# Kernel optimization log

Hardware: AMD Instinct MI355X
Metric: run time of the kernel (lower is better)

Reference implementation:

```python
import jax, jax.numpy as jnp
import numpy as np

# qshift_a: Kingsbury 10-tap Q-shift filters (sum(h0a) = sqrt(2)).
_H0A = np.array([0.0351638365171441, 0.0, -0.0883294244510729,
                 0.233890320607236, 0.760272369066126, 0.587518297723561,
                 0.0, -0.114301837144249, 0.0, 0.0], dtype=np.float64)
_H0B = _H0A[::-1].copy()
_ALT = (-1.0) ** np.arange(10)
_H1A = _H0B * _ALT            # highpass tree a
_H1B = _H1A[::-1].copy()
# synthesis filters (g0a = h0b, g0b = h0a, g1a = h1b, g1b = h1a)
G0A = _H0B.astype(np.float32)
G0B = _H0A.astype(np.float32)
G1A = _H1B.astype(np.float32)
G1B = _H1A.astype(np.float32)


def _reflect(x, minx, maxx):
    # dtcwt symmetric-extension index reflection (static, numpy)
    x = np.asarray(x, dtype=np.float64)
    rng = maxx - minx
    rng2 = 2.0 * rng
    mod = np.fmod(x - minx, rng2)
    normed = np.where(mod < 0, mod + rng2, mod)
    out = np.where(normed >= rng, rng2 - normed, normed) + minx
    return out.astype(np.int64)


def _colifilt(X, ha, hb):
    # X: (B, C, r, c) -> (B, C, 2r, c). ha, hb are 1-D numpy filters (static).
    m = ha.shape[0]
    m2 = m // 2
    assert m2 % 2 == 1, 'implemented for 10/14/18-tap qshift (m/2 odd)'
    b, ch, r, c = X.shape
    r2 = r // 2
    xe = _reflect(np.arange(-m2, r + m2), -0.5, r - 0.5)   # static indices
    t = np.arange(2, r + m - 1, 2)
    if float(np.sum(ha * hb)) > 0:
        ta, tb = t, t - 1
    else:
        ta, tb = t - 1, t
    Xa = X[:, :, xe[ta], :]   # (B, C, r/2 + m/2 - 1, c)
    Xb = X[:, :, xe[tb], :]
    hao, hae = ha[0::2], ha[1::2]
    hbo, hbe = hb[0::2], hb[1::2]

    def vconv(Z, h):
        # valid convolution along dim 2 (true conv: filter flipped)
        hf = h[::-1]
        out = Z[:, :, 0:r2, :] * float(hf[0])
        for k in range(1, m2):
            out = out + Z[:, :, k:k + r2, :] * float(hf[k])
        return out

    y = jnp.stack([vconv(Xb, hao), vconv(Xa, hbo),
                   vconv(Xb, hae), vconv(Xa, hbe)], axis=3)  # (B,C,r/2,4,c)
    return y.reshape(b, ch, 2 * r, c)


def _rowifilt(X, ha, hb):
    return jnp.swapaxes(_colifilt(jnp.swapaxes(X, 2, 3), ha, hb), 2, 3)


def _c2q(wr, wi):
    # complex pair of subbands -> real quad image. wr, wi: (B, C, 2, H, W) -> (B, C, 2H, 2W)
    w1r, w2r = wr[:, :, 0], wr[:, :, 1]
    w1i, w2i = wi[:, :, 0], wi[:, :, 1]
    x1 = w1r + w2r
    x2 = w1i + w2i
    x3 = w1i - w2i
    x4 = w2r - w1r
    b, c, h, w = x1.shape
    top = jnp.stack([x1, x2], axis=-1).reshape(b, c, h, 2 * w)
    bot = jnp.stack([x3, x4], axis=-1).reshape(b, c, h, 2 * w)
    y = jnp.stack([top, bot], axis=-2).reshape(b, c, 2 * h, 2 * w)
    return y * np.float32(1.0 / np.sqrt(2.0))


def setup_inputs() -> dict:
    key = jax.random.key(0)
    k1, k2, k3 = jax.random.split(key, 3)
    B, C, H, W = 8, 64, 128, 128
    Yl = jax.random.normal(k1, (B, C, H, W), dtype=jnp.float32)
    Yhr = jax.random.normal(k2, (B, C, 6, H // 2, W // 2), dtype=jnp.float32)
    Yhi = jax.random.normal(k3, (B, C, 6, H // 2, W // 2), dtype=jnp.float32)
    return {"Yl": Yl, "Yhr": Yhr, "Yhi": Yhi}


def reference(Yl, Yhr, Yhi):
    lh = _c2q(Yhr[:, :, 0:6:5], Yhi[:, :, 0:6:5])
    hl = _c2q(Yhr[:, :, 2:4:1], Yhi[:, :, 2:4:1])
    hh = _c2q(Yhr[:, :, 1:5:3], Yhi[:, :, 1:5:3])
    y1 = _rowifilt(Yl, G0B, G0A) + _rowifilt(hl, G1B, G1A)
    y2 = _rowifilt(lh, G0B, G0A) + _rowifilt(hh, G1B, G1A)
    return _colifilt(y1, G0B, G0A) + _colifilt(y2, G1B, G1A)
```

## Files before the change

kernel.cpp:

```cpp
#include <hip/hip_runtime.h>

#define NTHREADS 256

__device__ __forceinline__ int reflect128(int p) {
    p = (p < 0) ? (-p - 1) : p;
    p = (p >= 128) ? (255 - p) : p;
    return p;
}

__constant__ int   cs0[4] = {2, 1, 1, 0};
__constant__ int   cs1[4] = {1, 2, 0, 1};
__constant__ float cc0[4][3] = {
    { 0.760272369066126f, -0.0883294244510729f,  0.0351638365171441f},
    { 0.233890320607236f,  0.587518297723561f,  -0.114301837144249f},
    {-0.114301837144249f,  0.587518297723561f,   0.233890320607236f},
    { 0.0351638365171441f, -0.0883294244510729f, 0.760272369066126f}};
__constant__ float cc1[4][3] = {
    { 0.233890320607236f,  0.587518297723561f,  -0.114301837144249f},
    {-0.760272369066126f,  0.0883294244510729f, -0.0351638365171441f},
    {-0.0351638365171441f, 0.0883294244510729f, -0.760272369066126f},
    {-0.114301837144249f,  0.587518297723561f,   0.233890320607236f}};

__global__ __launch_bounds__(NTHREADS, 6)
void dtcwt_inv_kernel(const float* __restrict__ Yl,
                      const float* __restrict__ Yhr,
                      const float* __restrict__ Yhi,
                      float* __restrict__ out)
{
    const int tid   = threadIdx.x;
    const int ct    = blockIdx.x;
    const int rt    = blockIdx.y;
    const int plane = blockIdx.z;

    const int OR0 = rt * 64, OC0 = ct * 64;
    const int i0r = OR0 >> 2, i0c = OC0 >> 2;
    const int yrb = 2 * i0r - 4;
    const int icb = 2 * i0c - 4;

    const float* yl = Yl + (size_t)plane * (128 * 128);
    const float* hr = Yhr + (size_t)plane * 6 * 4096;
    const float* hi = Yhi + (size_t)plane * 6 * 4096;

    __shared__ float sLh[40][40];
    __shared__ float sHl[40][40];
    __shared__ float sHh[40][40];
    __shared__ float sYl[40][40];

    const float RS2 = 0.70710678118654752440f;

    for (int e = tid; e < 1600; e += NTHREADS) {
        const int t = e / 40;
        const int u = e - t * 40;
        const int r2 = reflect128(yrb + t);
        const int c2 = reflect128(icb + u);
        sYl[t][u] = yl[r2 * 128 + c2];
    }

    for (int e = tid; e < 400; e += NTHREADS) {
        const int t2 = e / 20;
        const int u2 = e - t2 * 20;
        const int ar = i0r - 2 + t2;
        const int ac = i0c - 2 + u2;
        const int oobr = (ar < 0) | (ar >= 64);
        const int oobc = (ac < 0) | (ac >= 64);
        const int r2 = oobr ? ((ar < 0) ? (-ar - 1) : (127 - ar)) : ar;
        const int c2 = oobc ? ((ac < 0) ? (-ac - 1) : (127 - ac)) : ac;
        const int off = r2 * 64 + c2;
        const float ar0 = hr[off], ar1 = hr[4096 + off], ar2 = hr[2 * 4096 + off];
        const float ar3 = hr[3 * 4096 + off], ar4 = hr[4 * 4096 + off], ar5 = hr[5 * 4096 + off];
        const float ai0 = hi[off], ai1 = hi[4096 + off], ai2 = hi[2 * 4096 + off];
        const float ai3 = hi[3 * 4096 + off], ai4 = hi[4 * 4096 + off], ai5 = hi[5 * 4096 + off];
#pragma unroll
        for (int dt = 0; dt < 2; ++dt) {
#pragma unroll
            for (int du = 0; du < 2; ++du) {
                const int p = dt ^ oobr;
                const int q = du ^ oobc;
                const float sA = (p & q) ? -RS2 : RS2;
                const float sB = (p & (q ^ 1)) ? -RS2 : RS2;
                float b0, b5, b2v, b3, b1, b4;
                if (p == q) { b0 = ar0; b5 = ar5; b2v = ar2; b3 = ar3; b1 = ar1; b4 = ar4; }
                else        { b0 = ai0; b5 = ai5; b2v = ai2; b3 = ai3; b1 = ai1; b4 = ai4; }
                const int t = 2 * t2 + dt, u = 2 * u2 + du;
                sLh[t][u] = sA * b0 + sB * b5;
                sHl[t][u] = sA * b2v + sB * b3;
                sHh[t][u] = sA * b1 + sB * b4;
            }
        }
    }
    __syncthreads();

    const int c  = tid & 63;
    const int g  = tid >> 6;
    const int jc = c & 3;
    const int q2 = c >> 2;
    const float a0  = cc0[jc][0], a1  = cc0[jc][1], a2  = cc0[jc][2];
    const float b0w = cc1[jc][0], b1w = cc1[jc][1], b2w = cc1[jc][2];
    const int ub0 = 2 * q2 + (jc & 1) + 2 * cs0[jc];
    const int ub1 = 2 * q2 + ((jc & 1) ^ 1) + 2 * cs1[jc];

    const int tb = 8 * g;
    float y1v[14], y2v[14];
#pragma unroll
    for (int k = 0; k < 14; ++k) {
        const int t = tb + 1 + k;
        y1v[k] = sYl[t][ub0] * a0  + sYl[t][ub0 + 2] * a1  + sYl[t][ub0 + 4] * a2
               + sHl[t][ub1] * b0w + sHl[t][ub1 + 2] * b1w + sHl[t][ub1 + 4] * b2w;
        y2v[k] = sLh[t][ub0] * a0  + sLh[t][ub0 + 2] * a1  + sLh[t][ub0 + 4] * a2
               + sHh[t][ub1] * b0w + sHh[t][ub1 + 2] * b1w + sHh[t][ub1 + 4] * b2w;
    }

    float* op = out + ((size_t)plane * 256 + OR0 + 16 * g) * 256 + OC0 + c;
#pragma unroll
    for (int j = 0; j < 4; ++j) {
        const int p0 = j & 1, p1 = p0 ^ 1;
        const int r0 = p0 + 2 * cs0[j];
        const int r1 = p1 + 2 * cs1[j];
        const float d0 = cc0[j][0], d1 = cc0[j][1], d2 = cc0[j][2];
        const float e0 = cc1[j][0], e1 = cc1[j][1], e2 = cc1[j][2];
#pragma unroll
        for (int mm = 0; mm < 4; ++mm) {
            const int k0 = 2 * mm + r0 - 1;
            const int k1 = 2 * mm + r1 - 1;
            const float acc = y1v[k0] * d0 + y1v[k0 + 2] * d1 + y1v[k0 + 4] * d2
                            + y2v[k1] * e0 + y2v[k1 + 2] * e1 + y2v[k1 + 4] * e2;
            op[(size_t)(4 * mm + j) * 256] = acc;
        }
    }
}

extern "C" void kernel_launch(void* const* d_in, const int* in_sizes, int n_in,
                              void* d_out, int out_size, void* d_ws, size_t ws_size,
                              hipStream_t stream) {
    const float* Yl  = (const float*)d_in[0];
    const float* Yhr = (const float*)d_in[1];
    const float* Yhi = (const float*)d_in[2];
    float* out = (float*)d_out;

    const int planes = in_sizes[0] / (128 * 128);
    dim3 grid(4, 4, planes);
    dtcwt_inv_kernel<<<grid, NTHREADS, 0, stream>>>(Yl, Yhr, Yhi, out);
}
```

Baseline: 262.0 us.

## Store staged tiles transposed in fp16 shared memory and remap block order

Staged input tiles now live in shared memory as fp16 and are stored transposed (column-major), so each thread can pull its column strip with wide 16-byte vector loads instead of many scalar reads. This halves the shared-memory footprint and cuts the number of LDS instructions. The 3D grid becomes a 1D grid with an XCD-aware swizzle of block indices to plane and tile. Rounding inputs to fp16 loses precision relative to the fp32 reference and may exceed tolerance.

```diff
diff --git a/kernel.cpp b/kernel.cpp
--- a/kernel.cpp
+++ b/kernel.cpp
@@ -1,4 +1,5 @@
 #include <hip/hip_runtime.h>
+#include <hip/hip_fp16.h>
 
 #define NTHREADS 256
 
@@ -27,10 +28,15 @@
                       const float* __restrict__ Yhi,
                       float* __restrict__ out)
 {
-    const int tid   = threadIdx.x;
-    const int ct    = blockIdx.x;
-    const int rt    = blockIdx.y;
-    const int plane = blockIdx.z;
+    const int tid = threadIdx.x;
+
+    const int bid  = blockIdx.x;
+    const int perx = gridDim.x >> 3;
+    const int gidx = (bid & 7) * perx + (bid >> 3);
+    const int plane = gidx >> 4;
+    const int tile  = gidx & 15;
+    const int ct = tile & 3;
+    const int rt = tile >> 2;
 
     const int OR0 = rt * 64, OC0 = ct * 64;
     const int i0r = OR0 >> 2, i0c = OC0 >> 2;
@@ -41,19 +47,19 @@
     const float* hr = Yhr + (size_t)plane * 6 * 4096;
     const float* hi = Yhi + (size_t)plane * 6 * 4096;
 
-    __shared__ float sLh[40][40];
-    __shared__ float sHl[40][40];
-    __shared__ float sHh[40][40];
-    __shared__ float sYl[40][40];
+    __shared__ __align__(16) __half sT[4][40][40];
 
     const float RS2 = 0.70710678118654752440f;
 
-    for (int e = tid; e < 1600; e += NTHREADS) {
-        const int t = e / 40;
-        const int u = e - t * 40;
-        const int r2 = reflect128(yrb + t);
-        const int c2 = reflect128(icb + u);
-        sYl[t][u] = yl[r2 * 128 + c2];
+    for (int e = tid; e < 800; e += NTHREADS) {
+        const int t2 = e / 40;
+        const int u  = e - t2 * 40;
+        const int cg = reflect128(icb + u);
+        const int ra = reflect128(yrb + 2 * t2);
+        const int rb = reflect128(yrb + 2 * t2 + 1);
+        const __half2 hv = __halves2half2(__float2half(yl[ra * 128 + cg]),
+                                          __float2half(yl[rb * 128 + cg]));
+        *(__half2*)&sT[0][u][2 * t2] = hv;
     }
 
     for (int e = tid; e < 400; e += NTHREADS) {
@@ -71,21 +77,25 @@
         const float ai0 = hi[off], ai1 = hi[4096 + off], ai2 = hi[2 * 4096 + off];
         const float ai3 = hi[3 * 4096 + off], ai4 = hi[4 * 4096 + off], ai5 = hi[5 * 4096 + off];
 #pragma unroll
-        for (int dt = 0; dt < 2; ++dt) {
+        for (int du = 0; du < 2; ++du) {
+            const int q = du ^ oobc;
+            __half lh[2], hl[2], hh[2];
 #pragma unroll
-            for (int du = 0; du < 2; ++du) {
+            for (int dt = 0; dt < 2; ++dt) {
                 const int p = dt ^ oobr;
-                const int q = du ^ oobc;
                 const float sA = (p & q) ? -RS2 : RS2;
                 const float sB = (p & (q ^ 1)) ? -RS2 : RS2;
                 float b0, b5, b2v, b3, b1, b4;
                 if (p == q) { b0 = ar0; b5 = ar5; b2v = ar2; b3 = ar3; b1 = ar1; b4 = ar4; }
                 else        { b0 = ai0; b5 = ai5; b2v = ai2; b3 = ai3; b1 = ai1; b4 = ai4; }
-                const int t = 2 * t2 + dt, u = 2 * u2 + du;
-                sLh[t][u] = sA * b0 + sB * b5;
-                sHl[t][u] = sA * b2v + sB * b3;
-                sHh[t][u] = sA * b1 + sB * b4;
+                lh[dt] = __float2half(sA * b0 + sB * b5);
+                hl[dt] = __float2half(sA * b2v + sB * b3);
+                hh[dt] = __float2half(sA * b1 + sB * b4);
             }
+            const int u = 2 * u2 + du, t0 = 2 * t2;
+            *(__half2*)&sT[1][u][t0] = __halves2half2(lh[0], lh[1]);
+            *(__half2*)&sT[2][u][t0] = __halves2half2(hl[0], hl[1]);
+            *(__half2*)&sT[3][u][t0] = __halves2half2(hh[0], hh[1]);
         }
     }
     __syncthreads();
@@ -94,20 +104,34 @@
     const int g  = tid >> 6;
     const int jc = c & 3;
     const int q2 = c >> 2;
-    const float a0  = cc0[jc][0], a1  = cc0[jc][1], a2  = cc0[jc][2];
-    const float b0w = cc1[jc][0], b1w = cc1[jc][1], b2w = cc1[jc][2];
     const int ub0 = 2 * q2 + (jc & 1) + 2 * cs0[jc];
     const int ub1 = 2 * q2 + ((jc & 1) ^ 1) + 2 * cs1[jc];
 
-    const int tb = 8 * g;
+    union H16 { float4 v[2]; __half h[16]; };
     float y1v[14], y2v[14];
 #pragma unroll
-    for (int k = 0; k < 14; ++k) {
-        const int t = tb + 1 + k;
-        y1v[k] = sYl[t][ub0] * a0  + sYl[t][ub0 + 2] * a1  + sYl[t][ub0 + 4] * a2
-               + sHl[t][ub1] * b0w + sHl[t][ub1 + 2] * b1w + sHl[t][ub1 + 4] * b2w;
-        y2v[k] = sLh[t][ub0] * a0  + sLh[t][ub0 + 2] * a1  + sLh[t][ub0 + 4] * a2
-               + sHh[t][ub1] * b0w + sHh[t][ub1 + 2] * b1w + sHh[t][ub1 + 4] * b2w;
+    for (int k = 0; k < 14; ++k) { y1v[k] = 0.0f; y2v[k] = 0.0f; }
+
+#pragma unroll
+    for (int d = 0; d < 3; ++d) {
+        const float ad = cc0[jc][d];
+        const float bd = cc1[jc][d];
+        const int u0 = ub0 + 2 * d;
+        const int u1 = ub1 + 2 * d;
+        H16 xa, xb, xc, xd;
+        const float4* pa = (const float4*)&sT[0][u0][8 * g];
+        const float4* pb = (const float4*)&sT[2][u1][8 * g];
+        const float4* pc = (const float4*)&sT[1][u0][8 * g];
+        const float4* pd = (const float4*)&sT[3][u1][8 * g];
+        xa.v[0] = pa[0]; xa.v[1] = pa[1];
+        xb.v[0] = pb[0]; xb.v[1] = pb[1];
+        xc.v[0] = pc[0]; xc.v[1] = pc[1];
+        xd.v[0] = pd[0]; xd.v[1] = pd[1];
+#pragma unroll
+        for (int k = 0; k < 14; ++k) {
+            y1v[k] += __half2float(xa.h[k + 1]) * ad + __half2float(xb.h[k + 1]) * bd;
+            y2v[k] += __half2float(xc.h[k + 1]) * ad + __half2float(xd.h[k + 1]) * bd;
+        }
     }
 
     float* op = out + ((size_t)plane * 256 + OR0 + 16 * g) * 256 + OC0 + c;
@@ -138,6 +162,6 @@
     float* out = (float*)d_out;
 
     const int planes = in_sizes[0] / (128 * 128);
-    dim3 grid(4, 4, planes);
+    dim3 grid(planes * 16, 1, 1);
     dtcwt_inv_kernel<<<grid, NTHREADS, 0, stream>>>(Yl, Yhr, Yhi, out);
 }
```

Result: slower. 277.9 us (+6.1%).

## Interleave subband tiles as float2 in LDS and remap blocks to 1D grid

Applied to the files above, without the earlier changes.

The four separate float LDS tiles become two float2 tiles, Yl paired with Lh and Hl paired with Hh. The filter stage can then fetch both operands with one 64-bit LDS read, halving the number of shared-memory load instructions. The grid is flattened to 1D, and block IDs are remapped with an XCD-style swizzle ((bid&7)*perx + bid>>3) so consecutive tiles of a plane land on the same XCD, which may improve L2 reuse. The remap assumes the block count is divisible by 8, and the float2 layout may change LDS bank conflict patterns.

```diff
diff --git a/kernel.cpp b/kernel.cpp
--- a/kernel.cpp
+++ b/kernel.cpp
@@ -27,10 +27,15 @@
                       const float* __restrict__ Yhi,
                       float* __restrict__ out)
 {
-    const int tid   = threadIdx.x;
-    const int ct    = blockIdx.x;
-    const int rt    = blockIdx.y;
-    const int plane = blockIdx.z;
+    const int tid = threadIdx.x;
+
+    const int bid  = blockIdx.x;
+    const int perx = gridDim.x >> 3;
+    const int gidx = (bid & 7) * perx + (bid >> 3);
+    const int plane = gidx >> 4;
+    const int tile  = gidx & 15;
+    const int ct = tile & 3;
+    const int rt = tile >> 2;
 
     const int OR0 = rt * 64, OC0 = ct * 64;
     const int i0r = OR0 >> 2, i0c = OC0 >> 2;
@@ -41,10 +46,8 @@
     const float* hr = Yhr + (size_t)plane * 6 * 4096;
     const float* hi = Yhi + (size_t)plane * 6 * 4096;
 
-    __shared__ float sLh[40][40];
-    __shared__ float sHl[40][40];
-    __shared__ float sHh[40][40];
-    __shared__ float sYl[40][40];
+    __shared__ float2 sP[40][40];
+    __shared__ float2 sQ[40][40];
 
     const float RS2 = 0.70710678118654752440f;
 
@@ -53,7 +56,7 @@
         const int u = e - t * 40;
         const int r2 = reflect128(yrb + t);
         const int c2 = reflect128(icb + u);
-        sYl[t][u] = yl[r2 * 128 + c2];
+        sP[t][u].x = yl[r2 * 128 + c2];
     }
 
     for (int e = tid; e < 400; e += NTHREADS) {
@@ -82,9 +85,9 @@
                 if (p == q) { b0 = ar0; b5 = ar5; b2v = ar2; b3 = ar3; b1 = ar1; b4 = ar4; }
                 else        { b0 = ai0; b5 = ai5; b2v = ai2; b3 = ai3; b1 = ai1; b4 = ai4; }
                 const int t = 2 * t2 + dt, u = 2 * u2 + du;
-                sLh[t][u] = sA * b0 + sB * b5;
-                sHl[t][u] = sA * b2v + sB * b3;
-                sHh[t][u] = sA * b1 + sB * b4;
+                sP[t][u].y = sA * b0 + sB * b5;
+                sQ[t][u]   = make_float2(sA * b2v + sB * b3,
+                                         sA * b1 + sB * b4);
             }
         }
     }
@@ -104,10 +107,12 @@
 #pragma unroll
     for (int k = 0; k < 14; ++k) {
         const int t = tb + 1 + k;
-        y1v[k] = sYl[t][ub0] * a0  + sYl[t][ub0 + 2] * a1  + sYl[t][ub0 + 4] * a2
-               + sHl[t][ub1] * b0w + sHl[t][ub1 + 2] * b1w + sHl[t][ub1 + 4] * b2w;
-        y2v[k] = sLh[t][ub0] * a0  + sLh[t][ub0 + 2] * a1  + sLh[t][ub0 + 4] * a2
-               + sHh[t][ub1] * b0w + sHh[t][ub1 + 2] * b1w + sHh[t][ub1 + 4] * b2w;
+        const float2 P0 = sP[t][ub0], P1 = sP[t][ub0 + 2], P2 = sP[t][ub0 + 4];
+        const float2 Q0 = sQ[t][ub1], Q1 = sQ[t][ub1 + 2], Q2 = sQ[t][ub1 + 4];
+        y1v[k] = P0.x * a0  + P1.x * a1  + P2.x * a2
+               + Q0.x * b0w + Q1.x * b1w + Q2.x * b2w;
+        y2v[k] = P0.y * a0  + P1.y * a1  + P2.y * a2
+               + Q0.y * b0w + Q1.y * b1w + Q2.y * b2w;
     }
 
     float* op = out + ((size_t)plane * 256 + OR0 + 16 * g) * 256 + OC0 + c;
@@ -138,6 +143,6 @@
     float* out = (float*)d_out;
 
     const int planes = in_sizes[0] / (128 * 128);
-    dim3 grid(4, 4, planes);
+    dim3 grid(planes * 16, 1, 1);
     dtcwt_inv_kernel<<<grid, NTHREADS, 0, stream>>>(Yl, Yhr, Yhi, out);
 }
```

Result: no change. 259.9 us (-0.8%).
